# Kernel optimization log

Hardware: AMD Instinct MI355X
Metric: run time of the kernel (lower is better)

Reference implementation:

```python
import jax, jax.numpy as jnp
import numpy as np

EMBED_DIM = 1024
NUM_HEADS = 16
HEAD_DIM = EMBED_DIM // NUM_HEADS


def setup_inputs() -> dict:
    key = jax.random.key(0)
    k1, k2, k3 = jax.random.split(key, 3)
    B, S = 2, 2048
    x = jax.random.normal(k1, (B, S, EMBED_DIM), dtype=jnp.float32)
    # Xavier-uniform-style init for dense kernels
    lim_qkv = float(np.sqrt(6.0 / (EMBED_DIM + 3 * EMBED_DIM)))
    w_qkv = jax.random.uniform(k2, (EMBED_DIM, 3 * EMBED_DIM), jnp.float32, -lim_qkv, lim_qkv)
    b_qkv = jnp.zeros((3 * EMBED_DIM,), jnp.float32)
    lim_out = float(np.sqrt(6.0 / (EMBED_DIM + EMBED_DIM)))
    w_out = jax.random.uniform(k3, (EMBED_DIM, EMBED_DIM), jnp.float32, -lim_out, lim_out)
    b_out = jnp.zeros((EMBED_DIM,), jnp.float32)
    return {"x": x, "w_qkv": w_qkv, "b_qkv": b_qkv, "w_out": w_out, "b_out": b_out}


def reference(x, w_qkv, b_qkv, w_out, b_out):
    B, S, E = x.shape
    qkv = x @ w_qkv + b_qkv                       # [B, S, 3E]
    qkv = qkv.reshape(B, S, NUM_HEADS, 3 * HEAD_DIM)
    qkv = qkv.transpose(0, 2, 1, 3)               # [B, H, S, 3*dh]
    q, k, v = jnp.split(qkv, 3, axis=-1)          # each [B, H, S, dh]
    scale = 1.0 / jnp.sqrt(jnp.asarray(HEAD_DIM, x.dtype))
    logits = jnp.einsum('bhqd,bhkd->bhqk', q, k) * scale  # [B, H, S, S]
    attn = jax.nn.softmax(logits, axis=-1)
    vals = jnp.einsum('bhqk,bhkd->bhqd', attn, v)  # [B, H, S, dh]
    vals = vals.transpose(0, 2, 1, 3).reshape(B, S, E)
    return vals @ w_out + b_out
```

## Files before the change

### kernel.cpp

```cpp
#include <hip/hip_runtime.h>
#include <cstdint>

typedef unsigned short u16;
typedef unsigned int u32;
typedef __attribute__((ext_vector_type(8))) short bf16x8;
typedef __attribute__((ext_vector_type(4))) float f32x4;
typedef __attribute__((ext_vector_type(16))) float f32x16;
typedef __attribute__((ext_vector_type(2))) unsigned int u32x2;

#if __has_builtin(__builtin_amdgcn_exp2f)
#define EXP2(x) __builtin_amdgcn_exp2f(x)
#else
#define EXP2(x) exp2f(x)
#endif

__device__ __forceinline__ u16 f2bf(float f) {
  unsigned u = __float_as_uint(f);
  u += 0x7fffu + ((u >> 16) & 1u);
  return (u16)(u >> 16);
}
__device__ __forceinline__ u32 pk_bf16(float lo, float hi) {
#if __has_builtin(__builtin_amdgcn_cvt_pk_bf16_f32)
  auto r = __builtin_amdgcn_cvt_pk_bf16_f32(lo, hi);
  return __builtin_bit_cast(u32, r);
#else
  u32 a = __float_as_uint(lo), b = __float_as_uint(hi);
  a += 0x7fffu + ((a >> 16) & 1u);
  b += 0x7fffu + ((b >> 16) & 1u);
  return (a >> 16) | (b & 0xffff0000u);
#endif
}

__device__ __forceinline__ void plane32swap(u32 x, u32 y, u32& r0, u32& r1) {
#if __has_builtin(__builtin_amdgcn_permlane32_swap)
  u32x2 r = __builtin_amdgcn_permlane32_swap(x, y, false, false);
  r0 = r[0]; r1 = r[1];
#else
  const u32 xs = (u32)__shfl_xor((int)x, 32, 64);
  const u32 ys = (u32)__shfl_xor((int)y, 32, 64);
  const bool hi = (threadIdx.x & 32) != 0;
  r0 = hi ? ys : x;
  r1 = hi ? y : xs;
#endif
}

__device__ __forceinline__ void async_load16(const void* g, void* l) {
  typedef const __attribute__((address_space(1))) void* gp_t;
  typedef __attribute__((address_space(3))) void* lp_t;
  __builtin_amdgcn_global_load_lds((gp_t)(uintptr_t)g, (lp_t)(uintptr_t)l, 16, 0, 0);
}

__global__ __launch_bounds__(256) void preprocess(
    const float* __restrict__ x, u16* __restrict__ xb,
    const float* __restrict__ wqkv, u16* __restrict__ dqkv,
    const float* __restrict__ wout, u16* __restrict__ dout)
{
  __shared__ u16 tile[64][65];
  const int t = threadIdx.x;
  const int bx = blockIdx.x;
  if (bx < 2048) {
    const size_t i = ((size_t)bx * 256 + t) * 8;
    const float4 a = *(const float4*)(x + i);
    const float4 b = *(const float4*)(x + i + 4);
    union { u16 u[8]; bf16x8 v; } p;
    p.u[0] = f2bf(a.x); p.u[1] = f2bf(a.y); p.u[2] = f2bf(a.z); p.u[3] = f2bf(a.w);
    p.u[4] = f2bf(b.x); p.u[5] = f2bf(b.y); p.u[6] = f2bf(b.z); p.u[7] = f2bf(b.w);
    *(bf16x8*)(xb + i) = p.v;
    return;
  }
  const int tb = bx - 2048;
  const int bxx = tb & 63, byy = tb >> 6;
  const bool isOut = bxx >= 48;
  const float* src = isOut ? wout : wqkv;
  u16* dst = isOut ? dout : dqkv;
  const int cols = isOut ? 1024 : 3072;
  const int rows = 1024;
  const int tc = (isOut ? (bxx - 48) : bxx) * 64;
  const int tr = byy * 64;
  const int r = t >> 2, c0 = (t & 3) * 16;
  const float* sp = src + (size_t)(tr + r) * cols + tc + c0;
#pragma unroll
  for (int i = 0; i < 16; i += 4) {
    const float4 v = *(const float4*)(sp + i);
    tile[r][c0 + i + 0] = f2bf(v.x);
    tile[r][c0 + i + 1] = f2bf(v.y);
    tile[r][c0 + i + 2] = f2bf(v.z);
    tile[r][c0 + i + 3] = f2bf(v.w);
  }
  __syncthreads();
  u16* dp = dst + (size_t)(tc + r) * rows + tr + c0;
#pragma unroll
  for (int i = 0; i < 16; ++i) dp[i] = tile[c0 + i][r];
}

__global__ __launch_bounds__(256) void gemm_qkv(
    const u16* __restrict__ A, const u16* __restrict__ Bt, const float* __restrict__ bias,
    u16* __restrict__ Qp, u16* __restrict__ Kp, u16* __restrict__ Vtp)
{
  const int Kd = 1024;
  __shared__ __align__(16) u16 As[2][128 * 32];
  __shared__ __align__(16) u16 Bs[2][128 * 32];
  const int t = threadIdx.x;
  const int lane = t & 63, wave = t >> 6;
  const int quad = lane >> 4, m16 = lane & 15;
  const int mb = blockIdx.y * 128, nb = blockIdx.x * 128;
  const int wr = (wave & 1) * 64, wc = (wave >> 1) * 64;

  const int seg = (nb + wc) >> 6;
  const int h = seg / 3;
  const int which = seg - 3 * h;
  const bool isV = (which == 2);

  const int srow = t >> 2;
  const int scol = (t & 3) * 8;
  const u16* Ag0 = A + (size_t)(mb + srow) * Kd + scol;
  const u16* Ag1 = Ag0 + (size_t)64 * Kd;
  const u16* Bg0 = Bt + (size_t)(nb + srow) * Kd + scol;
  const u16* Bg1 = Bg0 + (size_t)64 * Kd;
  const int aoff = t * 8;

  f32x4 acc[4][4] = {};

#define GPRE(k0, B)                                                          \
  do {                                                                       \
    async_load16(Ag0 + (k0), &As[B][aoff]);                                  \
    async_load16(Ag1 + (k0), &As[B][aoff + 2048]);                           \
    async_load16(Bg0 + (k0), &Bs[B][aoff]);                                  \
    async_load16(Bg1 + (k0), &Bs[B][aoff + 2048]);                           \
  } while (0)

#define GSTEP(B)                                                             \
  do {                                                                       \
    bf16x8 af[4], bfr[4];                                                    \
    _Pragma("unroll")                                                        \
    for (int i = 0; i < 4; ++i)                                              \
      af[i] = *(const bf16x8*)(&As[B][(wr + i * 16 + m16) * 32 + quad * 8]); \
    _Pragma("unroll")                                                        \
    for (int i = 0; i < 4; ++i)                                              \
      bfr[i] = *(const bf16x8*)(&Bs[B][(wc + i * 16 + m16) * 32 + quad * 8]); \
    if (isV) {                                                               \
      _Pragma("unroll")                                                      \
      for (int i = 0; i < 4; ++i)                                            \
        _Pragma("unroll")                                                    \
        for (int j = 0; j < 4; ++j)                                          \
          acc[i][j] = __builtin_amdgcn_mfma_f32_16x16x32_bf16(bfr[i], af[j], acc[i][j], 0, 0, 0); \
    } else {                                                                 \
      _Pragma("unroll")                                                      \
      for (int i = 0; i < 4; ++i)                                            \
        _Pragma("unroll")                                                    \
        for (int j = 0; j < 4; ++j)                                          \
          acc[i][j] = __builtin_amdgcn_mfma_f32_16x16x32_bf16(af[i], bfr[j], acc[i][j], 0, 0, 0); \
    }                                                                        \
  } while (0)

  GPRE(0, 0);
  __syncthreads();
  for (int k0 = 0; k0 < Kd; k0 += 64) {
    GPRE(k0 + 32, 1);
    GSTEP(0);
    __syncthreads();
    if (k0 + 64 < Kd) GPRE(k0 + 64, 0);
    GSTEP(1);
    __syncthreads();
  }
#undef GPRE
#undef GSTEP

  const int b = mb >> 11;
  const size_t bh64 = (size_t)((b << 4) | h);

  if (isV) {
    const int sIbase = (mb & 2047) + wr;
    u16* dstV = Vtp + bh64 * 64 * 2048;
#pragma unroll
    for (int i = 0; i < 4; ++i)
#pragma unroll
      for (int r = 0; r < 4; ++r) {
        const int d = i * 16 + quad * 4 + r;
        const float bv = bias[nb + wc + d];
        u16* rp = dstV + (size_t)d * 2048 + sIbase;
#pragma unroll
        for (int j = 0; j < 4; ++j)
          rp[j * 16 + m16] = f2bf(acc[i][j][r] + bv);
      }
  } else {
    u16* dstP = (which == 0) ? Qp : Kp;
    const float qs = (which == 0) ? 0.18033688011112042f : 1.0f;
#pragma unroll
    for (int j = 0; j < 4; ++j) {
      const int base = nb + wc + j * 16;
      const float bv = bias[base + m16];
      const int d = (base & 63) + m16;
#pragma unroll
      for (int i = 0; i < 4; ++i)
#pragma unroll
        for (int r = 0; r < 4; ++r) {
          const int row = mb + wr + i * 16 + quad * 4 + r;
          const int sI = row & 2047;
          dstP[(bh64 * 2048 + sI) * 64 + d] = f2bf((acc[i][j][r] + bv) * qs);
        }
    }
  }
}

__global__ __launch_bounds__(256) void gemm_out(
    const u16* __restrict__ A, const u16* __restrict__ Bt, const float* __restrict__ bias,
    float* __restrict__ Outp)
{
  const int Kd = 1024;
  __shared__ __align__(16) u16 As[2][64 * 32];
  __shared__ __align__(16) u16 Bs[2][128 * 32];
  const int t = threadIdx.x;
  const int lane = t & 63, wave = t >> 6;
  const int quad = lane >> 4, m16 = lane & 15;
  const int mb = blockIdx.y * 64, nb = blockIdx.x * 128;
  const int wr = (wave & 1) * 32, wc = (wave >> 1) * 64;

  const int srow = t >> 2;
  const int scol = (t & 3) * 8;
  const u16* Ag0 = A + (size_t)(mb + srow) * Kd + scol;
  const u16* Bg0 = Bt + (size_t)(nb + srow) * Kd + scol;
  const u16* Bg1 = Bg0 + (size_t)64 * Kd;
  const int aoff = t * 8;

  f32x4 acc[2][4] = {};

#define OPRE(k0, B)                                                          \
  do {                                                                       \
    async_load16(Ag0 + (k0), &As[B][aoff]);                                  \
    async_load16(Bg0 + (k0), &Bs[B][aoff]);                                  \
    async_load16(Bg1 + (k0), &Bs[B][aoff + 2048]);                           \
  } while (0)

#define OSTEP(B)                                                             \
  do {                                                                       \
    bf16x8 af[2], bfr[4];                                                    \
    _Pragma("unroll")                                                        \
    for (int i = 0; i < 2; ++i)                                              \
      af[i] = *(const bf16x8*)(&As[B][(wr + i * 16 + m16) * 32 + quad * 8]); \
    _Pragma("unroll")                                                        \
    for (int j = 0; j < 4; ++j)                                              \
      bfr[j] = *(const bf16x8*)(&Bs[B][(wc + j * 16 + m16) * 32 + quad * 8]); \
    _Pragma("unroll")                                                        \
    for (int i = 0; i < 2; ++i)                                              \
      _Pragma("unroll")                                                      \
      for (int j = 0; j < 4; ++j)                                            \
        acc[i][j] = __builtin_amdgcn_mfma_f32_16x16x32_bf16(af[i], bfr[j], acc[i][j], 0, 0, 0); \
  } while (0)

  OPRE(0, 0);
  __syncthreads();
  for (int k0 = 0; k0 < Kd; k0 += 64) {
    OPRE(k0 + 32, 1);
    OSTEP(0);
    __syncthreads();
    if (k0 + 64 < Kd) OPRE(k0 + 64, 0);
    OSTEP(1);
    __syncthreads();
  }
#undef OPRE
#undef OSTEP

#pragma unroll
  for (int j = 0; j < 4; ++j) {
    const int col = nb + wc + j * 16 + m16;
    const float bv = bias[col];
#pragma unroll
    for (int i = 0; i < 2; ++i)
#pragma unroll
      for (int r = 0; r < 4; ++r) {
        const int row = mb + wr + i * 16 + quad * 4 + r;
        Outp[(size_t)row * 1024 + col] = acc[i][j][r] + bv;
      }
  }
}

__global__ __launch_bounds__(256) void flash_attn(
    const u16* __restrict__ Q, const u16* __restrict__ K, const u16* __restrict__ Vt,
    u16* __restrict__ O)
{
  const int S = 2048;
  __shared__ __align__(16) u16 Kl[2][64 * 64];
  __shared__ __align__(16) u16 Vl[2][64 * 64];
  const int t = threadIdx.x;
  const int lane = t & 63, w = t >> 6;
  const int l31 = lane & 31, hi = lane >> 5;

  const int f = blockIdx.x;
  const int wi = f >> 3;
  const int bh = (f & 7) + 8 * (wi & 3);
  const int q0 = (wi >> 2) * 128;

  const u16* Qb = Q + (size_t)bh * S * 64;
  const u16* Kb = K + (size_t)bh * S * 64;
  const u16* Vb = Vt + (size_t)bh * 64 * S;

  bf16x8 qf[4];
#pragma unroll
  for (int dc = 0; dc < 4; ++dc)
    qf[dc] = *(const bf16x8*)(Qb + (size_t)(q0 + w * 32 + l31) * 64 + dc * 16 + hi * 8);

  const u16* Kg[2]; const u16* Vg[2]; int soff[2];
#pragma unroll
  for (int l = 0; l < 2; ++l) {
    const int idx = l * 256 + t;
    const int row = idx >> 3, slot = idx & 7;
    const int sg = slot ^ (row & 7);
    Kg[l] = Kb + row * 64 + sg * 8;
    Vg[l] = Vb + (size_t)row * S + sg * 8;
    soff[l] = idx * 8;
  }

  f32x16 ot[2] = {};
  float lr4[4] = {0.f, 0.f, 0.f, 0.f};

#define PREFETCH(kvp, B)                                                     \
  do {                                                                       \
    _Pragma("unroll")                                                        \
    for (int l = 0; l < 2; ++l) async_load16(Kg[l] + (kvp) * 64, &Kl[B][soff[l]]); \
    _Pragma("unroll")                                                        \
    for (int l = 0; l < 2; ++l) async_load16(Vg[l] + (kvp), &Vl[B][soff[l]]);      \
  } while (0)

#define STEP(B)                                                              \
  do {                                                                       \
    bf16x8 pa[4];                                                            \
    _Pragma("unroll")                                                        \
    for (int kt = 0; kt < 2; ++kt) {                                         \
      f32x16 st = {0.f,0.f,0.f,0.f, 0.f,0.f,0.f,0.f,                         \
                   0.f,0.f,0.f,0.f, 0.f,0.f,0.f,0.f};                        \
      const int kvr = kt * 32 + l31;                                         \
      const u16* krow = &Kl[B][kvr * 64];                                    \
      _Pragma("unroll")                                                      \
      for (int dc = 0; dc < 4; ++dc) {                                       \
        const bf16x8 kb = *(const bf16x8*)(krow + (((dc * 2 + hi) ^ (kvr & 7)) * 8)); \
        st = __builtin_amdgcn_mfma_f32_32x32x16_bf16(kb, qf[dc], st, 0, 0, 0); \
      }                                                                      \
      float p[16];                                                           \
      _Pragma("unroll")                                                      \
      for (int r = 0; r < 16; ++r) { p[r] = EXP2(st[r]); lr4[r & 3] += p[r]; } \
      _Pragma("unroll")                                                      \
      for (int cc = 0; cc < 2; ++cc) {                                       \
        union { u32 u[4]; bf16x8 v; } fr;                                    \
        _Pragma("unroll")                                                    \
        for (int i = 0; i < 2; ++i) {                                        \
          const u32 xx = pk_bf16(p[8 * cc + 2 * i + 0], p[8 * cc + 2 * i + 1]); \
          const u32 yy = pk_bf16(p[8 * cc + 2 * i + 4], p[8 * cc + 2 * i + 5]); \
          u32 r0, r1;                                                        \
          plane32swap(xx, yy, r0, r1);                                       \
          fr.u[i] = r0; fr.u[2 + i] = r1;                                    \
        }                                                                    \
        pa[kt * 2 + cc] = fr.v;                                              \
      }                                                                      \
    }                                                                        \
    _Pragma("unroll")                                                        \
    for (int c = 0; c < 4; ++c) {                                            \
      _Pragma("unroll")                                                      \
      for (int dt = 0; dt < 2; ++dt) {                                       \
        const int dr = dt * 32 + l31;                                        \
        const bf16x8 va = *(const bf16x8*)(&Vl[B][dr * 64] + (((c * 2 + hi) ^ (dr & 7)) * 8)); \
        ot[dt] = __builtin_amdgcn_mfma_f32_32x32x16_bf16(va, pa[c], ot[dt], 0, 0, 0); \
      }                                                                      \
    }                                                                        \
  } while (0)

  PREFETCH(0, 0);
  __syncthreads();

  for (int kv0 = 0; kv0 < S; kv0 += 128) {
    PREFETCH(kv0 + 64, 1);
    STEP(0);
    __syncthreads();
    if (kv0 + 128 < S) PREFETCH(kv0 + 128, 0);
    STEP(1);
    __syncthreads();
  }
#undef PREFETCH
#undef STEP

  float l = lr4[0] + lr4[1] + lr4[2] + lr4[3];
  l += __shfl_xor(l, 32, 64);
  const float inv = 1.0f / l;
  const int b = bh >> 4, h = bh & 15;
  const int q = q0 + w * 32 + l31;
  u16* base = O + ((size_t)b * 2048 + q) * 1024 + h * 64;
#pragma unroll
  for (int dt = 0; dt < 2; ++dt)
#pragma unroll
    for (int g4 = 0; g4 < 4; ++g4) {
      const u32 lo = pk_bf16(ot[dt][4 * g4 + 0] * inv, ot[dt][4 * g4 + 1] * inv);
      const u32 h2 = pk_bf16(ot[dt][4 * g4 + 2] * inv, ot[dt][4 * g4 + 3] * inv);
      *(uint2*)(base + dt * 32 + 8 * g4 + 4 * hi) = make_uint2(lo, h2);
    }
}

extern "C" void kernel_launch(void* const* d_in, const int* in_sizes, int n_in,
                              void* d_out, int out_size, void* d_ws, size_t ws_size,
                              hipStream_t stream)
{
  const float* x     = (const float*)d_in[0];
  const float* w_qkv = (const float*)d_in[1];
  const float* b_qkv = (const float*)d_in[2];
  const float* w_out = (const float*)d_in[3];
  const float* b_out = (const float*)d_in[4];
  float* out = (float*)d_out;

  u16* ws     = (u16*)d_ws;
  u16* xb     = ws;
  u16* WtQKV  = xb + 4194304;
  u16* WtOut  = WtQKV + 3145728;
  u16* Qm     = WtOut + 1048576;
  u16* Km     = Qm + 4194304;
  u16* Vtm    = Km + 4194304;
  u16* AO     = Vtm + 4194304;

  preprocess<<<3072, 256, 0, stream>>>(x, xb, w_qkv, WtQKV, w_out, WtOut);
  gemm_qkv<<<dim3(24, 32), 256, 0, stream>>>(xb, WtQKV, b_qkv, Qm, Km, Vtm);
  flash_attn<<<512, 256, 0, stream>>>(Qm, Km, Vtm, AO);
  gemm_out<<<dim3(8, 64), 256, 0, stream>>>(AO, WtOut, b_out, out);
}
```

Before: 188.2 us.

## Split flash attention KV range across two wave groups and reduce via LDS

Doubles the attention block to 512 threads. Two groups of four waves each process half of the key/value sequence, each with its own double-buffered LDS tiles. At the end the second group writes its partial outputs and row sums to shared memory, and the first group adds them, normalises and stores. This is split-K parallelism inside a block, meant to raise wave occupancy and shorten each wave's serial loop over KV. In exchange it doubles LDS per block and adds a final reduction and barrier. Correctness relies on the softmax having no running max, so the partial sums can simply be added.

```diff
diff --git a/kernel.cpp b/kernel.cpp
--- a/kernel.cpp
+++ b/kernel.cpp
@@ -275,16 +275,20 @@
   }
 }
 
-__global__ __launch_bounds__(256) void flash_attn(
+__global__ __launch_bounds__(512) void flash_attn(
     const u16* __restrict__ Q, const u16* __restrict__ K, const u16* __restrict__ Vt,
     u16* __restrict__ O)
 {
   const int S = 2048;
-  __shared__ __align__(16) u16 Kl[2][64 * 64];
-  __shared__ __align__(16) u16 Vl[2][64 * 64];
+  __shared__ __align__(16) u16 SH[32768];
+  u16* const KlF = SH;
+  u16* const VlF = SH + 16384;
   const int t = threadIdx.x;
   const int lane = t & 63, w = t >> 6;
   const int l31 = lane & 31, hi = lane >> 5;
+  const int wq = w & 3;
+  const int half = w >> 2;
+  const int hoff = half * 8192;
 
   const int f = blockIdx.x;
   const int wi = f >> 3;
@@ -298,39 +302,44 @@
   bf16x8 qf[4];
 #pragma unroll
   for (int dc = 0; dc < 4; ++dc)
-    qf[dc] = *(const bf16x8*)(Qb + (size_t)(q0 + w * 32 + l31) * 64 + dc * 16 + hi * 8);
-
+    qf[dc] = *(const bf16x8*)(Qb + (size_t)(q0 + wq * 32 + l31) * 64 + dc * 16 + hi * 8);
+
+  const int tidx = t & 255;
   const u16* Kg[2]; const u16* Vg[2]; int soff[2];
 #pragma unroll
   for (int l = 0; l < 2; ++l) {
-    const int idx = l * 256 + t;
+    const int idx = l * 256 + tidx;
     const int row = idx >> 3, slot = idx & 7;
     const int sg = slot ^ (row & 7);
-    Kg[l] = Kb + row * 64 + sg * 8;
-    Vg[l] = Vb + (size_t)row * S + sg * 8;
+    Kg[l] = Kb + (size_t)(half * 1024 + row) * 64 + sg * 8;
+    Vg[l] = Vb + (size_t)row * S + half * 1024 + sg * 8;
     soff[l] = idx * 8;
   }
 
   f32x16 ot[2] = {};
   float lr4[4] = {0.f, 0.f, 0.f, 0.f};
 
-#define PREFETCH(kvp, B)                                                     \
-  do {                                                                       \
-    _Pragma("unroll")                                                        \
-    for (int l = 0; l < 2; ++l) async_load16(Kg[l] + (kvp) * 64, &Kl[B][soff[l]]); \
-    _Pragma("unroll")                                                        \
-    for (int l = 0; l < 2; ++l) async_load16(Vg[l] + (kvp), &Vl[B][soff[l]]);      \
+#define PRE(tile, B)                                                         \
+  do {                                                                       \
+    _Pragma("unroll")                                                        \
+    for (int l = 0; l < 2; ++l)                                              \
+      async_load16(Kg[l] + (size_t)(tile) * 4096, KlF + hoff + (B) * 4096 + soff[l]); \
+    _Pragma("unroll")                                                        \
+    for (int l = 0; l < 2; ++l)                                              \
+      async_load16(Vg[l] + (tile) * 64, VlF + hoff + (B) * 4096 + soff[l]);  \
   } while (0)
 
 #define STEP(B)                                                              \
   do {                                                                       \
+    const u16* kb_ = KlF + hoff + (B) * 4096;                                \
+    const u16* vb_ = VlF + hoff + (B) * 4096;                                \
     bf16x8 pa[4];                                                            \
     _Pragma("unroll")                                                        \
     for (int kt = 0; kt < 2; ++kt) {                                         \
       f32x16 st = {0.f,0.f,0.f,0.f, 0.f,0.f,0.f,0.f,                         \
                    0.f,0.f,0.f,0.f, 0.f,0.f,0.f,0.f};                        \
       const int kvr = kt * 32 + l31;                                         \
-      const u16* krow = &Kl[B][kvr * 64];                                    \
+      const u16* krow = kb_ + kvr * 64;                                      \
       _Pragma("unroll")                                                      \
       for (int dc = 0; dc < 4; ++dc) {                                       \
         const bf16x8 kb = *(const bf16x8*)(krow + (((dc * 2 + hi) ^ (kvr & 7)) * 8)); \
@@ -358,40 +367,60 @@
       _Pragma("unroll")                                                      \
       for (int dt = 0; dt < 2; ++dt) {                                       \
         const int dr = dt * 32 + l31;                                        \
-        const bf16x8 va = *(const bf16x8*)(&Vl[B][dr * 64] + (((c * 2 + hi) ^ (dr & 7)) * 8)); \
+        const bf16x8 va = *(const bf16x8*)(vb_ + dr * 64 + (((c * 2 + hi) ^ (dr & 7)) * 8)); \
         ot[dt] = __builtin_amdgcn_mfma_f32_32x32x16_bf16(va, pa[c], ot[dt], 0, 0, 0); \
       }                                                                      \
     }                                                                        \
   } while (0)
 
-  PREFETCH(0, 0);
+  PRE(0, 0);
   __syncthreads();
 
-  for (int kv0 = 0; kv0 < S; kv0 += 128) {
-    PREFETCH(kv0 + 64, 1);
+  for (int tp = 0; tp < 16; tp += 2) {
+    PRE(tp + 1, 1);
     STEP(0);
     __syncthreads();
-    if (kv0 + 128 < S) PREFETCH(kv0 + 128, 0);
+    if (tp + 2 < 16) PRE(tp + 2, 0);
     STEP(1);
     __syncthreads();
   }
-#undef PREFETCH
+#undef PRE
 #undef STEP
 
   float l = lr4[0] + lr4[1] + lr4[2] + lr4[3];
   l += __shfl_xor(l, 32, 64);
-  const float inv = 1.0f / l;
-  const int b = bh >> 4, h = bh & 15;
-  const int q = q0 + w * 32 + l31;
-  u16* base = O + ((size_t)b * 2048 + q) * 1024 + h * 64;
-#pragma unroll
-  for (int dt = 0; dt < 2; ++dt)
-#pragma unroll
-    for (int g4 = 0; g4 < 4; ++g4) {
-      const u32 lo = pk_bf16(ot[dt][4 * g4 + 0] * inv, ot[dt][4 * g4 + 1] * inv);
-      const u32 h2 = pk_bf16(ot[dt][4 * g4 + 2] * inv, ot[dt][4 * g4 + 3] * inv);
-      *(uint2*)(base + dt * 32 + 8 * g4 + 4 * hi) = make_uint2(lo, h2);
-    }
+
+  float* const smemF = (float*)SH;
+  if (half == 1) {
+#pragma unroll
+    for (int dt = 0; dt < 2; ++dt)
+#pragma unroll
+      for (int r = 0; r < 16; ++r)
+        smemF[wq * 2112 + (dt * 16 + r) * 64 + lane] = ot[dt][r];
+    smemF[wq * 2112 + 2048 + lane] = l;
+  }
+  __syncthreads();
+  if (half == 0) {
+    l += smemF[wq * 2112 + 2048 + lane];
+#pragma unroll
+    for (int dt = 0; dt < 2; ++dt)
+#pragma unroll
+      for (int r = 0; r < 16; ++r)
+        ot[dt][r] += smemF[wq * 2112 + (dt * 16 + r) * 64 + lane];
+
+    const float inv = 1.0f / l;
+    const int b = bh >> 4, h = bh & 15;
+    const int q = q0 + wq * 32 + l31;
+    u16* base = O + ((size_t)b * 2048 + q) * 1024 + h * 64;
+#pragma unroll
+    for (int dt = 0; dt < 2; ++dt)
+#pragma unroll
+      for (int g4 = 0; g4 < 4; ++g4) {
+        const u32 lo = pk_bf16(ot[dt][4 * g4 + 0] * inv, ot[dt][4 * g4 + 1] * inv);
+        const u32 h2 = pk_bf16(ot[dt][4 * g4 + 2] * inv, ot[dt][4 * g4 + 3] * inv);
+        *(uint2*)(base + dt * 32 + 8 * g4 + 4 * hi) = make_uint2(lo, h2);
+      }
+  }
 }
 
 extern "C" void kernel_launch(void* const* d_in, const int* in_sizes, int n_in,
@@ -416,6 +445,6 @@
 
   preprocess<<<3072, 256, 0, stream>>>(x, xb, w_qkv, WtQKV, w_out, WtOut);
   gemm_qkv<<<dim3(24, 32), 256, 0, stream>>>(xb, WtQKV, b_qkv, Qm, Km, Vtm);
-  flash_attn<<<512, 256, 0, stream>>>(Qm, Km, Vtm, AO);
+  flash_attn<<<512, 512, 0, stream>>>(Qm, Km, Vtm, AO);
   gemm_out<<<dim3(8, 64), 256, 0, stream>>>(AO, WtOut, b_out, out);
 }
```

Measured after the change: 185.9 us. Within noise of the previous version (-1.2%).

## Load K/V tiles directly from global memory into registers, dropping LDS staging

Applied to the files above, without the earlier changes.

The flash attention kernel no longer stages K and V tiles through shared memory with async loads and barriers. Each wave now loads its K and V MFMA fragments straight from global memory into registers, double-buffering K across tiles and dropping all __syncthreads. This removes LDS traffic and barrier stalls, but the four waves in a block each fetch the same K/V data through cache, and the register footprint grows, which may lower occupancy.

```diff
diff --git a/kernel.cpp b/kernel.cpp
--- a/kernel.cpp
+++ b/kernel.cpp
@@ -280,8 +280,6 @@
     u16* __restrict__ O)
 {
   const int S = 2048;
-  __shared__ __align__(16) u16 Kl[2][64 * 64];
-  __shared__ __align__(16) u16 Vl[2][64 * 64];
   const int t = threadIdx.x;
   const int lane = t & 63, w = t >> 6;
   const int l31 = lane & 31, hi = lane >> 5;
@@ -300,42 +298,40 @@
   for (int dc = 0; dc < 4; ++dc)
     qf[dc] = *(const bf16x8*)(Qb + (size_t)(q0 + w * 32 + l31) * 64 + dc * 16 + hi * 8);
 
-  const u16* Kg[2]; const u16* Vg[2]; int soff[2];
-#pragma unroll
-  for (int l = 0; l < 2; ++l) {
-    const int idx = l * 256 + t;
-    const int row = idx >> 3, slot = idx & 7;
-    const int sg = slot ^ (row & 7);
-    Kg[l] = Kb + row * 64 + sg * 8;
-    Vg[l] = Vb + (size_t)row * S + sg * 8;
-    soff[l] = idx * 8;
-  }
+  const u16* const Kp0 = Kb + (size_t)l31 * 64 + hi * 8;
+  const u16* const Vp0 = Vb + (size_t)l31 * S + hi * 8;
 
   f32x16 ot[2] = {};
   float lr4[4] = {0.f, 0.f, 0.f, 0.f};
-
-#define PREFETCH(kvp, B)                                                     \
-  do {                                                                       \
-    _Pragma("unroll")                                                        \
-    for (int l = 0; l < 2; ++l) async_load16(Kg[l] + (kvp) * 64, &Kl[B][soff[l]]); \
-    _Pragma("unroll")                                                        \
-    for (int l = 0; l < 2; ++l) async_load16(Vg[l] + (kvp), &Vl[B][soff[l]]);      \
-  } while (0)
-
-#define STEP(B)                                                              \
-  do {                                                                       \
-    bf16x8 pa[4];                                                            \
+  bf16x8 kA[8], kB[8], vv[8], pa[4];
+
+#define LOADK(ARR, tile)                                                     \
+  do {                                                                       \
+    _Pragma("unroll")                                                        \
+    for (int kt = 0; kt < 2; ++kt)                                           \
+      _Pragma("unroll")                                                      \
+      for (int dc = 0; dc < 4; ++dc)                                         \
+        ARR[kt * 4 + dc] = *(const bf16x8*)(Kp0 + (size_t)((tile) * 64 + kt * 32) * 64 + dc * 16); \
+  } while (0)
+
+#define LOADV(tile)                                                          \
+  do {                                                                       \
+    _Pragma("unroll")                                                        \
+    for (int dt = 0; dt < 2; ++dt)                                           \
+      _Pragma("unroll")                                                      \
+      for (int c = 0; c < 4; ++c)                                            \
+        vv[dt * 4 + c] = *(const bf16x8*)(Vp0 + (size_t)dt * 32 * S + (tile) * 64 + c * 16); \
+  } while (0)
+
+#define QKT_SM(KARR)                                                         \
+  do {                                                                       \
     _Pragma("unroll")                                                        \
     for (int kt = 0; kt < 2; ++kt) {                                         \
       f32x16 st = {0.f,0.f,0.f,0.f, 0.f,0.f,0.f,0.f,                         \
                    0.f,0.f,0.f,0.f, 0.f,0.f,0.f,0.f};                        \
-      const int kvr = kt * 32 + l31;                                         \
-      const u16* krow = &Kl[B][kvr * 64];                                    \
-      _Pragma("unroll")                                                      \
-      for (int dc = 0; dc < 4; ++dc) {                                       \
-        const bf16x8 kb = *(const bf16x8*)(krow + (((dc * 2 + hi) ^ (kvr & 7)) * 8)); \
-        st = __builtin_amdgcn_mfma_f32_32x32x16_bf16(kb, qf[dc], st, 0, 0, 0); \
-      }                                                                      \
+      _Pragma("unroll")                                                      \
+      for (int dc = 0; dc < 4; ++dc)                                         \
+        st = __builtin_amdgcn_mfma_f32_32x32x16_bf16(KARR[kt * 4 + dc], qf[dc], st, 0, 0, 0); \
       float p[16];                                                           \
       _Pragma("unroll")                                                      \
       for (int r = 0; r < 16; ++r) { p[r] = EXP2(st[r]); lr4[r & 3] += p[r]; } \
@@ -353,30 +349,32 @@
         pa[kt * 2 + cc] = fr.v;                                              \
       }                                                                      \
     }                                                                        \
-    _Pragma("unroll")                                                        \
-    for (int c = 0; c < 4; ++c) {                                            \
-      _Pragma("unroll")                                                      \
-      for (int dt = 0; dt < 2; ++dt) {                                       \
-        const int dr = dt * 32 + l31;                                        \
-        const bf16x8 va = *(const bf16x8*)(&Vl[B][dr * 64] + (((c * 2 + hi) ^ (dr & 7)) * 8)); \
-        ot[dt] = __builtin_amdgcn_mfma_f32_32x32x16_bf16(va, pa[c], ot[dt], 0, 0, 0); \
-      }                                                                      \
-    }                                                                        \
-  } while (0)
-
-  PREFETCH(0, 0);
-  __syncthreads();
-
-  for (int kv0 = 0; kv0 < S; kv0 += 128) {
-    PREFETCH(kv0 + 64, 1);
-    STEP(0);
-    __syncthreads();
-    if (kv0 + 128 < S) PREFETCH(kv0 + 128, 0);
-    STEP(1);
-    __syncthreads();
-  }
-#undef PREFETCH
-#undef STEP
+  } while (0)
+
+#define PV()                                                                 \
+  do {                                                                       \
+    _Pragma("unroll")                                                        \
+    for (int c = 0; c < 4; ++c)                                              \
+      _Pragma("unroll")                                                      \
+      for (int dt = 0; dt < 2; ++dt)                                         \
+        ot[dt] = __builtin_amdgcn_mfma_f32_32x32x16_bf16(vv[dt * 4 + c], pa[c], ot[dt], 0, 0, 0); \
+  } while (0)
+
+  LOADK(kA, 0);
+  for (int tp = 0; tp < 32; tp += 2) {
+    LOADV(tp);
+    LOADK(kB, tp + 1);
+    QKT_SM(kA);
+    PV();
+    LOADV(tp + 1);
+    if (tp + 2 < 32) LOADK(kA, tp + 2);
+    QKT_SM(kB);
+    PV();
+  }
+#undef LOADK
+#undef LOADV
+#undef QKT_SM
+#undef PV
 
   float l = lr4[0] + lr4[1] + lr4[2] + lr4[3];
   l += __shfl_xor(l, 32, 64);
```

New measurement: 254.9 us. +35.5%, slower.
